# Kernel tuning notes

Measured on AMD Instinct MI355X. Metric: run time of the kernel, lower is better.

Reference implementation:

```python
import jax, jax.numpy as jnp
import numpy as np

ATOMF_LEN = 82
EDGE_DIM = 6
HIDDEN = 10
GNN_DEPTH = 2
N_NODES = 200000
N_EDGES = 6400000


def _lrelu(x):
    return jax.nn.leaky_relu(x, negative_slope=0.1)


def setup_inputs() -> dict:
    key = jax.random.key(0)
    ks = jax.random.split(key, 7)
    vertex = jax.random.normal(ks[0], (N_NODES, ATOMF_LEN), dtype=jnp.float32)
    edge_feat = jax.random.normal(ks[1], (N_EDGES, EDGE_DIM), dtype=jnp.float32)
    src = jax.random.randint(ks[2], (N_EDGES,), 0, N_NODES, dtype=jnp.int32)
    dst = jax.random.randint(ks[3], (N_EDGES,), 0, N_NODES, dtype=jnp.int32)
    # kaiming-uniform-ish init scale (fan_in based)
    weight_init = jax.random.uniform(ks[4], (ATOMF_LEN, HIDDEN), dtype=jnp.float32,
                                     minval=-1.0, maxval=1.0) * (np.sqrt(6.0 / ATOMF_LEN))
    gather_weight = jax.random.uniform(ks[5], (HIDDEN + EDGE_DIM, HIDDEN), dtype=jnp.float32,
                                       minval=-1.0, maxval=1.0) * (np.sqrt(6.0 / (HIDDEN + EDGE_DIM)))
    update_weight = jax.random.uniform(ks[6], (2 * HIDDEN, HIDDEN), dtype=jnp.float32,
                                       minval=-1.0, maxval=1.0) * (np.sqrt(6.0 / (2 * HIDDEN)))
    return {"vertex": vertex, "edge_feat": edge_feat, "src": src, "dst": dst,
            "weight_init": weight_init, "gather_weight": gather_weight,
            "update_weight": update_weight}


def reference(vertex, edge_feat, src, dst, weight_init, gather_weight, update_weight):
    # embedding_: leaky_relu(mm(x, W), 0.1)
    h = _lrelu(vertex @ weight_init)  # [N, HIDDEN]
    n_nodes = vertex.shape[0]
    for _ in range(GNN_DEPTH):
        # gather: per-edge message from source node hidden + edge features
        msg = _lrelu(jnp.concatenate([h[src], edge_feat], axis=1) @ gather_weight)  # [E, HIDDEN]
        # scatter-sum aggregation onto destination nodes
        agg = jax.ops.segment_sum(msg, dst, num_segments=n_nodes)  # [N, HIDDEN]
        # update: combine current hidden with aggregated messages
        h = _lrelu(jnp.concatenate([h, agg], axis=1) @ update_weight)  # [N, HIDDEN]
    return h
```

## Files before the change

### kernel.cpp

```cpp
#include <hip/hip_runtime.h>

#define ATOMF 82
#define EDGE_DIM 6
#define HIDDEN 10
#define ZPAD 16

__device__ __forceinline__ float lrelu(float x) { return x > 0.f ? x : 0.1f * x; }

__device__ __forceinline__ unsigned int f2bf(float f) {
    unsigned int u = __float_as_uint(f);
    return (u + 0x7fffu + ((u >> 16) & 1u)) >> 16;
}
__device__ __forceinline__ float bf2f(unsigned int b) {
    return __uint_as_float(b << 16);
}

__global__ void embed_kernel(const float* __restrict__ vertex,
                             const float* __restrict__ W,
                             const float* __restrict__ GW,
                             float* __restrict__ h, unsigned short* __restrict__ z,
                             int n_nodes) {
    __shared__ float w[ATOMF * HIDDEN];
    __shared__ float gwh[HIDDEN * HIDDEN];
    for (int i = threadIdx.x; i < ATOMF * HIDDEN; i += blockDim.x) w[i] = W[i];
    for (int i = threadIdx.x; i < HIDDEN * HIDDEN; i += blockDim.x) gwh[i] = GW[i];
    __syncthreads();
    int node = blockIdx.x * blockDim.x + threadIdx.x;
    if (node >= n_nodes) return;
    const float2* v = (const float2*)(vertex + (long)node * ATOMF);
    float acc[HIDDEN];
#pragma unroll
    for (int j = 0; j < HIDDEN; j++) acc[j] = 0.f;
#pragma unroll 2
    for (int k2 = 0; k2 < ATOMF / 2; k2++) {
        float2 t = v[k2];
#pragma unroll
        for (int j = 0; j < HIDDEN; j++) acc[j] += t.x * w[(2 * k2) * HIDDEN + j];
#pragma unroll
        for (int j = 0; j < HIDDEN; j++) acc[j] += t.y * w[(2 * k2 + 1) * HIDDEN + j];
    }
    float ho[HIDDEN];
    float* out = h + (long)node * HIDDEN;
#pragma unroll
    for (int j = 0; j < HIDDEN; j++) { ho[j] = lrelu(acc[j]); out[j] = ho[j]; }
    float zv[HIDDEN];
#pragma unroll
    for (int j = 0; j < HIDDEN; j++) zv[j] = 0.f;
#pragma unroll
    for (int k = 0; k < HIDDEN; k++) {
        float x = ho[k];
#pragma unroll
        for (int j = 0; j < HIDDEN; j++) zv[j] += x * gwh[k * HIDDEN + j];
    }
    unsigned int* zq = (unsigned int*)(z + (size_t)node * ZPAD);
    int4 pk;
    pk.x = (int)(f2bf(zv[0]) | (f2bf(zv[1]) << 16));
    pk.y = (int)(f2bf(zv[2]) | (f2bf(zv[3]) << 16));
    pk.z = (int)(f2bf(zv[4]) | (f2bf(zv[5]) << 16));
    pk.w = (int)(f2bf(zv[6]) | (f2bf(zv[7]) << 16));
    *(int4*)zq = pk;
    zq[4] = f2bf(zv[8]) | (f2bf(zv[9]) << 16);
}

__global__ void count_pos_kernel(const int* __restrict__ dst, int* __restrict__ counts,
                                 unsigned short* __restrict__ pos, long n_edges) {
    long e0 = ((long)blockIdx.x * blockDim.x + threadIdx.x) * 4;
    if (e0 + 3 < n_edges) {
        int4 d = *(const int4*)(dst + e0);
        ushort4 p;
        p.x = (unsigned short)atomicAdd(&counts[d.x], 1);
        p.y = (unsigned short)atomicAdd(&counts[d.y], 1);
        p.z = (unsigned short)atomicAdd(&counts[d.z], 1);
        p.w = (unsigned short)atomicAdd(&counts[d.w], 1);
        *(ushort4*)(pos + e0) = p;
    } else {
        for (long e = e0; e < n_edges; e++)
            pos[e] = (unsigned short)atomicAdd(&counts[dst[e]], 1);
    }
}

__global__ __launch_bounds__(1024) void scan_block_sums(const int* __restrict__ counts,
                                                        int* __restrict__ partials, int n) {
    __shared__ int ws[16];
    int i = blockIdx.x * 1024 + threadIdx.x;
    int v = (i < n) ? counts[i] : 0;
    int lane = threadIdx.x & 63, wid = threadIdx.x >> 6;
    int s = v;
#pragma unroll
    for (int off = 32; off > 0; off >>= 1) s += __shfl_down(s, off, 64);
    if (lane == 0) ws[wid] = s;
    __syncthreads();
    if (threadIdx.x == 0) {
        int t = 0;
#pragma unroll
        for (int k = 0; k < 16; k++) t += ws[k];
        partials[blockIdx.x] = t;
    }
}
__global__ __launch_bounds__(1024) void scan_partials(int* __restrict__ partials, int nb) {
    __shared__ int wsum[16];
    int lane = threadIdx.x & 63, wid = threadIdx.x >> 6;
    int v = (threadIdx.x < nb) ? partials[threadIdx.x] : 0;
    int incl = v;
#pragma unroll
    for (int off = 1; off < 64; off <<= 1) {
        int t = __shfl_up(incl, off, 64);
        if (lane >= off) incl += t;
    }
    if (lane == 63) wsum[wid] = incl;
    __syncthreads();
    if (wid == 0 && lane < 16) {
        int wv = wsum[lane];
        int wincl = wv;
#pragma unroll
        for (int off = 1; off < 16; off <<= 1) {
            int t = __shfl_up(wincl, off, 64);
            if (lane >= off) wincl += t;
        }
        wsum[lane] = wincl - wv;
    }
    __syncthreads();
    if (threadIdx.x < nb) partials[threadIdx.x] = wsum[wid] + (incl - v);
}
__global__ __launch_bounds__(1024) void scan_final(const int* __restrict__ counts,
                                                   const int* __restrict__ partials,
                                                   int* __restrict__ offsets, int n) {
    __shared__ int wsum[16];
    int i = blockIdx.x * 1024 + threadIdx.x;
    int v = (i < n) ? counts[i] : 0;
    int lane = threadIdx.x & 63, wid = threadIdx.x >> 6;
    int incl = v;
#pragma unroll
    for (int off = 1; off < 64; off <<= 1) {
        int t = __shfl_up(incl, off, 64);
        if (lane >= off) incl += t;
    }
    if (lane == 63) wsum[wid] = incl;
    __syncthreads();
    if (wid == 0 && lane < 16) {
        int wv = wsum[lane];
        int wincl = wv;
#pragma unroll
        for (int off = 1; off < 16; off <<= 1) {
            int t = __shfl_up(wincl, off, 64);
            if (lane >= off) wincl += t;
        }
        wsum[lane] = wincl - wv;
    }
    __syncthreads();
    if (i <= n) offsets[i] = partials[blockIdx.x] + wsum[wid] + (incl - v);
}

__global__ void scatter_rec_kernel(const int* __restrict__ src, const int* __restrict__ dst,
                                   const float* __restrict__ ef,
                                   const unsigned short* __restrict__ pos,
                                   const int* __restrict__ offsets,
                                   int4* __restrict__ rec, long n_edges) {
    long e = (long)blockIdx.x * blockDim.x + threadIdx.x;
    if (e >= n_edges) return;
    int d = dst[e];
    int q = offsets[d] + (int)pos[e];
    const float2* er = (const float2*)(ef + e * (long)EDGE_DIM);
    float2 a = er[0], b = er[1], c = er[2];
    int4 r;
    r.x = src[e];
    r.y = (int)(f2bf(a.x) | (f2bf(a.y) << 16));
    r.z = (int)(f2bf(b.x) | (f2bf(b.y) << 16));
    r.w = (int)(f2bf(c.x) | (f2bf(c.y) << 16));
    rec[q] = r;
}

__global__ __launch_bounds__(256) void gather_update_kernel(
    const float* __restrict__ h_in, const unsigned short* __restrict__ z_in,
    const int4* __restrict__ rec, const int* __restrict__ offsets,
    const float* __restrict__ GW, const float* __restrict__ UW,
    float* __restrict__ h_out, unsigned short* __restrict__ z_out,
    int n_nodes, int write_z) {
    __shared__ float gwh[HIDDEN * HIDDEN];
    __shared__ float gwe[EDGE_DIM * HIDDEN];
    __shared__ float uw[2 * HIDDEN * HIDDEN];
    for (int i = threadIdx.x; i < HIDDEN * HIDDEN; i += 256) gwh[i] = GW[i];
    for (int i = threadIdx.x; i < EDGE_DIM * HIDDEN; i += 256) gwe[i] = GW[HIDDEN * HIDDEN + i];
    for (int i = threadIdx.x; i < 2 * HIDDEN * HIDDEN; i += 256) uw[i] = UW[i];
    __syncthreads();
    int group = threadIdx.x >> 4;
    int sub = threadIdx.x & 15;
    int node = blockIdx.x * 16 + group;
    if (node >= n_nodes) return;
    int off0 = offsets[node], off1 = offsets[node + 1];
    float acc[HIDDEN];
#pragma unroll
    for (int j = 0; j < HIDDEN; j++) acc[j] = 0.f;
    int p = off0 + sub;
    int4 r;
    if (p < off1) r = rec[p];
    while (p < off1) {
        int pn = p + 16;
        int4 rn = r;
        if (pn < off1) rn = rec[pn];
        const int* zq = (const int*)(z_in + (size_t)r.x * ZPAD);
        int4 za = *(const int4*)zq;
        int zb = zq[4];
        float ef[EDGE_DIM];
        unsigned int u0 = (unsigned int)r.y, u1 = (unsigned int)r.z, u2 = (unsigned int)r.w;
        ef[0] = bf2f(u0 & 0xffffu); ef[1] = bf2f(u0 >> 16);
        ef[2] = bf2f(u1 & 0xffffu); ef[3] = bf2f(u1 >> 16);
        ef[4] = bf2f(u2 & 0xffffu); ef[5] = bf2f(u2 >> 16);
        float m[HIDDEN];
#pragma unroll
        for (int j = 0; j < HIDDEN; j++) m[j] = 0.f;
#pragma unroll
        for (int k = 0; k < EDGE_DIM; k++) {
            float x = ef[k];
#pragma unroll
            for (int j = 0; j < HIDDEN; j++) m[j] += x * gwe[k * HIDDEN + j];
        }
        unsigned int z0 = (unsigned int)za.x, z1 = (unsigned int)za.y;
        unsigned int z2 = (unsigned int)za.z, z3 = (unsigned int)za.w, z4 = (unsigned int)zb;
        acc[0] += lrelu(m[0] + bf2f(z0 & 0xffffu));
        acc[1] += lrelu(m[1] + bf2f(z0 >> 16));
        acc[2] += lrelu(m[2] + bf2f(z1 & 0xffffu));
        acc[3] += lrelu(m[3] + bf2f(z1 >> 16));
        acc[4] += lrelu(m[4] + bf2f(z2 & 0xffffu));
        acc[5] += lrelu(m[5] + bf2f(z2 >> 16));
        acc[6] += lrelu(m[6] + bf2f(z3 & 0xffffu));
        acc[7] += lrelu(m[7] + bf2f(z3 >> 16));
        acc[8] += lrelu(m[8] + bf2f(z4 & 0xffffu));
        acc[9] += lrelu(m[9] + bf2f(z4 >> 16));
        r = rn; p = pn;
    }
#pragma unroll
    for (int j = 0; j < HIDDEN; j++) {
#pragma unroll
        for (int d = 8; d > 0; d >>= 1) acc[j] += __shfl_down(acc[j], d, 16);
    }
    if (sub == 0) {
        float in[2 * HIDDEN];
        const float2* hp = (const float2*)(h_in + (long)node * HIDDEN);
#pragma unroll
        for (int k = 0; k < 5; k++) { float2 t = hp[k]; in[2 * k] = t.x; in[2 * k + 1] = t.y; }
#pragma unroll
        for (int j = 0; j < HIDDEN; j++) in[HIDDEN + j] = acc[j];
        float o[HIDDEN];
#pragma unroll
        for (int j = 0; j < HIDDEN; j++) o[j] = 0.f;
#pragma unroll
        for (int k = 0; k < 2 * HIDDEN; k++) {
            float x = in[k];
#pragma unroll
            for (int j = 0; j < HIDDEN; j++) o[j] += x * uw[k * HIDDEN + j];
        }
        float ho[HIDDEN];
        float* outp = h_out + (long)node * HIDDEN;
#pragma unroll
        for (int j = 0; j < HIDDEN; j++) { ho[j] = lrelu(o[j]); outp[j] = ho[j]; }
        if (write_z) {
            float zv[HIDDEN];
#pragma unroll
            for (int j = 0; j < HIDDEN; j++) zv[j] = 0.f;
#pragma unroll
            for (int k = 0; k < HIDDEN; k++) {
                float x = ho[k];
#pragma unroll
                for (int j = 0; j < HIDDEN; j++) zv[j] += x * gwh[k * HIDDEN + j];
            }
            unsigned int* zq = (unsigned int*)(z_out + (size_t)node * ZPAD);
            int4 pk;
            pk.x = (int)(f2bf(zv[0]) | (f2bf(zv[1]) << 16));
            pk.y = (int)(f2bf(zv[2]) | (f2bf(zv[3]) << 16));
            pk.z = (int)(f2bf(zv[4]) | (f2bf(zv[5]) << 16));
            pk.w = (int)(f2bf(zv[6]) | (f2bf(zv[7]) << 16));
            *(int4*)zq = pk;
            zq[4] = f2bf(zv[8]) | (f2bf(zv[9]) << 16);
        }
    }
}

extern "C" void kernel_launch(void* const* d_in, const int* in_sizes, int n_in,
                              void* d_out, int out_size, void* d_ws, size_t ws_size,
                              hipStream_t stream) {
    const float* vertex    = (const float*)d_in[0];
    const float* edge_feat = (const float*)d_in[1];
    const int*   src       = (const int*)d_in[2];
    const int*   dst       = (const int*)d_in[3];
    const float* w_init    = (const float*)d_in[4];
    const float* gw        = (const float*)d_in[5];
    const float* uw        = (const float*)d_in[6];

    const int  n_nodes = in_sizes[0] / ATOMF;
    const long n_edges = (long)in_sizes[2];
    float* out = (float*)d_out;

    char* ws = (char*)d_ws;
    size_t o = 0;
    auto alloc = [&](size_t bytes) { char* p = ws + o; o = (o + bytes + 255) & ~(size_t)255; return p; };
    int*  counts   = (int*)alloc((size_t)(n_nodes + 1) * sizeof(int));
    int*  offsets  = (int*)alloc((size_t)(n_nodes + 1) * sizeof(int));
    int*  partials = (int*)alloc(2048 * sizeof(int));
    int4* rec      = (int4*)alloc((size_t)n_edges * sizeof(int4));
    size_t pos_bytes = (size_t)n_edges * sizeof(unsigned short);
    size_t tbl_bytes = (size_t)n_nodes * (2 * HIDDEN * sizeof(float) + 2 * ZPAD * sizeof(unsigned short));
    char* overlay = alloc(pos_bytes > tbl_bytes ? pos_bytes : tbl_bytes);
    unsigned short* pos = (unsigned short*)overlay;
    float*          h0  = (float*)overlay;
    float*          h1  = h0 + (size_t)n_nodes * HIDDEN;
    unsigned short* z0  = (unsigned short*)(h1 + (size_t)n_nodes * HIDDEN);
    unsigned short* z1  = z0 + (size_t)n_nodes * ZPAD;
    (void)ws_size;

    const int TB = 256;
    const int node_blocks = (n_nodes + TB - 1) / TB;
    const int edge_blocks = (int)((n_edges + TB - 1) / TB);
    const int cp_blocks   = (int)((n_edges / 4 + TB - 1) / TB);
    const int gu_blocks   = (n_nodes + 15) / 16;
    const int scan_blocks = (n_nodes + 1 + 1023) / 1024;

    hipMemsetAsync(counts, 0, (size_t)(n_nodes + 1) * sizeof(int), stream);
    count_pos_kernel<<<cp_blocks, TB, 0, stream>>>(dst, counts, pos, n_edges);
    scan_block_sums<<<scan_blocks, 1024, 0, stream>>>(counts, partials, n_nodes);
    scan_partials<<<1, 1024, 0, stream>>>(partials, scan_blocks);
    scan_final<<<scan_blocks, 1024, 0, stream>>>(counts, partials, offsets, n_nodes);
    scatter_rec_kernel<<<edge_blocks, TB, 0, stream>>>(src, dst, edge_feat, pos, offsets,
                                                       rec, n_edges);

    embed_kernel<<<node_blocks, TB, 0, stream>>>(vertex, w_init, gw, h0, z0, n_nodes);

    gather_update_kernel<<<gu_blocks, TB, 0, stream>>>(h0, z0, rec, offsets, gw, uw,
                                                       h1, z1, n_nodes, 1);
    gather_update_kernel<<<gu_blocks, TB, 0, stream>>>(h1, z1, rec, offsets, gw, uw,
                                                       out, z0, n_nodes, 0);
}
```

Before: 913.9 us.

## Privatize per-XCD destination counters to keep CSR-build atomics local

The counting pass now gives each XCD (read from the hardware XCC_ID register) its own copy of the per-node counters and issues workgroup-scoped relaxed atomics on that copy. The XCD id is packed into the high bits of the 16-bit position field. The scans sum the eight copies, and the final scan turns each copy into a per-XCD base offset that the scatter pass uses. This targets cross-die coherence traffic and contention on device-scope atomics, at the cost of eight times the counter memory and extra reads during the scan. It relies on per-XCD counts staying below 8192 per node, and on workgroup-scope atomics staying coherent within one XCD's L2.

```diff
diff --git a/kernel.cpp b/kernel.cpp
--- a/kernel.cpp
+++ b/kernel.cpp
@@ -4,6 +4,9 @@
 #define EDGE_DIM 6
 #define HIDDEN 10
 #define ZPAD 16
+#define NXCD 8
+#define POSBITS 13
+#define POSMASK 0x1fff
 
 __device__ __forceinline__ float lrelu(float x) { return x > 0.f ? x : 0.1f * x; }
 
@@ -13,6 +16,12 @@
 }
 __device__ __forceinline__ float bf2f(unsigned int b) {
     return __uint_as_float(b << 16);
+}
+
+__device__ __forceinline__ int xcc_id() {
+    unsigned int x;
+    asm("s_getreg_b32 %0, hwreg(HW_REG_XCC_ID)" : "=s"(x));
+    return (int)(x & (NXCD - 1));
 }
 
 __global__ void embed_kernel(const float* __restrict__ vertex,
@@ -62,28 +71,40 @@
     zq[4] = f2bf(zv[8]) | (f2bf(zv[9]) << 16);
 }
 
-__global__ void count_pos_kernel(const int* __restrict__ dst, int* __restrict__ counts,
-                                 unsigned short* __restrict__ pos, long n_edges) {
+__global__ void count_pos_kernel(const int* __restrict__ dst, int* __restrict__ counts8,
+                                 unsigned short* __restrict__ pos, int n_nodes, long n_edges) {
+    int xcc = xcc_id();
+    int* mycnt = counts8 + (size_t)xcc * (size_t)n_nodes;
+    unsigned int tag = (unsigned int)xcc << POSBITS;
     long e0 = ((long)blockIdx.x * blockDim.x + threadIdx.x) * 4;
     if (e0 + 3 < n_edges) {
         int4 d = *(const int4*)(dst + e0);
         ushort4 p;
-        p.x = (unsigned short)atomicAdd(&counts[d.x], 1);
-        p.y = (unsigned short)atomicAdd(&counts[d.y], 1);
-        p.z = (unsigned short)atomicAdd(&counts[d.z], 1);
-        p.w = (unsigned short)atomicAdd(&counts[d.w], 1);
+        p.x = (unsigned short)(tag | __hip_atomic_fetch_add(&mycnt[d.x], 1, __ATOMIC_RELAXED,
+                                                            __HIP_MEMORY_SCOPE_WORKGROUP));
+        p.y = (unsigned short)(tag | __hip_atomic_fetch_add(&mycnt[d.y], 1, __ATOMIC_RELAXED,
+                                                            __HIP_MEMORY_SCOPE_WORKGROUP));
+        p.z = (unsigned short)(tag | __hip_atomic_fetch_add(&mycnt[d.z], 1, __ATOMIC_RELAXED,
+                                                            __HIP_MEMORY_SCOPE_WORKGROUP));
+        p.w = (unsigned short)(tag | __hip_atomic_fetch_add(&mycnt[d.w], 1, __ATOMIC_RELAXED,
+                                                            __HIP_MEMORY_SCOPE_WORKGROUP));
         *(ushort4*)(pos + e0) = p;
     } else {
         for (long e = e0; e < n_edges; e++)
-            pos[e] = (unsigned short)atomicAdd(&counts[dst[e]], 1);
-    }
-}
-
-__global__ __launch_bounds__(1024) void scan_block_sums(const int* __restrict__ counts,
+            pos[e] = (unsigned short)(tag | __hip_atomic_fetch_add(&mycnt[dst[e]], 1, __ATOMIC_RELAXED,
+                                                                   __HIP_MEMORY_SCOPE_WORKGROUP));
+    }
+}
+
+__global__ __launch_bounds__(1024) void scan_block_sums(const int* __restrict__ counts8,
                                                         int* __restrict__ partials, int n) {
     __shared__ int ws[16];
     int i = blockIdx.x * 1024 + threadIdx.x;
-    int v = (i < n) ? counts[i] : 0;
+    int v = 0;
+    if (i < n) {
+#pragma unroll
+        for (int x = 0; x < NXCD; x++) v += counts8[(size_t)x * n + i];
+    }
     int lane = threadIdx.x & 63, wid = threadIdx.x >> 6;
     int s = v;
 #pragma unroll
@@ -122,12 +143,17 @@
     __syncthreads();
     if (threadIdx.x < nb) partials[threadIdx.x] = wsum[wid] + (incl - v);
 }
-__global__ __launch_bounds__(1024) void scan_final(const int* __restrict__ counts,
+__global__ __launch_bounds__(1024) void scan_final(int* __restrict__ counts8,
                                                    const int* __restrict__ partials,
                                                    int* __restrict__ offsets, int n) {
     __shared__ int wsum[16];
     int i = blockIdx.x * 1024 + threadIdx.x;
-    int v = (i < n) ? counts[i] : 0;
+    int c[NXCD];
+    int v = 0;
+    if (i < n) {
+#pragma unroll
+        for (int x = 0; x < NXCD; x++) { c[x] = counts8[(size_t)x * n + i]; v += c[x]; }
+    }
     int lane = threadIdx.x & 63, wid = threadIdx.x >> 6;
     int incl = v;
 #pragma unroll
@@ -148,18 +174,25 @@
         wsum[lane] = wincl - wv;
     }
     __syncthreads();
-    if (i <= n) offsets[i] = partials[blockIdx.x] + wsum[wid] + (incl - v);
+    int ex = partials[blockIdx.x] + wsum[wid] + (incl - v);
+    if (i < n) {
+        int b = ex;
+#pragma unroll
+        for (int x = 0; x < NXCD; x++) { int cx = c[x]; counts8[(size_t)x * n + i] = b; b += cx; }
+    }
+    if (i <= n) offsets[i] = ex;
 }
 
 __global__ void scatter_rec_kernel(const int* __restrict__ src, const int* __restrict__ dst,
                                    const float* __restrict__ ef,
                                    const unsigned short* __restrict__ pos,
-                                   const int* __restrict__ offsets,
-                                   int4* __restrict__ rec, long n_edges) {
+                                   const int* __restrict__ base8,
+                                   int4* __restrict__ rec, int n_nodes, long n_edges) {
     long e = (long)blockIdx.x * blockDim.x + threadIdx.x;
     if (e >= n_edges) return;
     int d = dst[e];
-    int q = offsets[d] + (int)pos[e];
+    unsigned int p = pos[e];
+    int q = base8[(size_t)(p >> POSBITS) * (size_t)n_nodes + d] + (int)(p & POSMASK);
     const float2* er = (const float2*)(ef + e * (long)EDGE_DIM);
     float2 a = er[0], b = er[1], c = er[2];
     int4 r;
@@ -294,7 +327,7 @@
     char* ws = (char*)d_ws;
     size_t o = 0;
     auto alloc = [&](size_t bytes) { char* p = ws + o; o = (o + bytes + 255) & ~(size_t)255; return p; };
-    int*  counts   = (int*)alloc((size_t)(n_nodes + 1) * sizeof(int));
+    int*  counts8  = (int*)alloc((size_t)NXCD * n_nodes * sizeof(int));
     int*  offsets  = (int*)alloc((size_t)(n_nodes + 1) * sizeof(int));
     int*  partials = (int*)alloc(2048 * sizeof(int));
     int4* rec      = (int4*)alloc((size_t)n_edges * sizeof(int4));
@@ -315,13 +348,13 @@
     const int gu_blocks   = (n_nodes + 15) / 16;
     const int scan_blocks = (n_nodes + 1 + 1023) / 1024;
 
-    hipMemsetAsync(counts, 0, (size_t)(n_nodes + 1) * sizeof(int), stream);
-    count_pos_kernel<<<cp_blocks, TB, 0, stream>>>(dst, counts, pos, n_edges);
-    scan_block_sums<<<scan_blocks, 1024, 0, stream>>>(counts, partials, n_nodes);
+    hipMemsetAsync(counts8, 0, (size_t)NXCD * n_nodes * sizeof(int), stream);
+    count_pos_kernel<<<cp_blocks, TB, 0, stream>>>(dst, counts8, pos, n_nodes, n_edges);
+    scan_block_sums<<<scan_blocks, 1024, 0, stream>>>(counts8, partials, n_nodes);
     scan_partials<<<1, 1024, 0, stream>>>(partials, scan_blocks);
-    scan_final<<<scan_blocks, 1024, 0, stream>>>(counts, partials, offsets, n_nodes);
-    scatter_rec_kernel<<<edge_blocks, TB, 0, stream>>>(src, dst, edge_feat, pos, offsets,
-                                                       rec, n_edges);
+    scan_final<<<scan_blocks, 1024, 0, stream>>>(counts8, partials, offsets, n_nodes);
+    scatter_rec_kernel<<<edge_blocks, TB, 0, stream>>>(src, dst, edge_feat, pos, counts8,
+                                                       rec, n_nodes, n_edges);
 
     embed_kernel<<<node_blocks, TB, 0, stream>>>(vertex, w_init, gw, h0, z0, n_nodes);
 
```

Result: slower. 961.7 us (+5.2%).

## Build CSR via two-pass bucketed radix partition instead of global atomics

Applied to the files above, without the earlier changes.

Replaces the per-edge global atomic counting and random scatter with a two-level partition. Edges are first histogrammed into 256-node buckets with shared-memory atomics and scattered by bucket. Each bucket is then sorted locally in shared memory to produce the CSR offsets and records. This is meant to cut contended global atomics and make the 16-byte record writes more local. In exchange it adds an extra pass over the records and needs extra workspace for the dst2 and rec_a buffers; if the workspace is too small it falls back to the old path.

```diff
diff --git a/kernel.cpp b/kernel.cpp
--- a/kernel.cpp
+++ b/kernel.cpp
@@ -4,6 +4,11 @@
 #define EDGE_DIM 6
 #define HIDDEN 10
 #define ZPAD 16
+
+#define BSHIFT 8
+#define MAXBUCK 1024
+#define NB1 1024
+#define MAXE3 16384
 
 __device__ __forceinline__ float lrelu(float x) { return x > 0.f ? x : 0.1f * x; }
 
@@ -60,6 +65,161 @@
     pk.w = (int)(f2bf(zv[6]) | (f2bf(zv[7]) << 16));
     *(int4*)zq = pk;
     zq[4] = f2bf(zv[8]) | (f2bf(zv[9]) << 16);
+}
+
+__global__ __launch_bounds__(256) void hist_kernel(const int* __restrict__ dst,
+                                                   int* __restrict__ hist,
+                                                   long n_edges, int nbuck) {
+    __shared__ int hl[MAXBUCK];
+    for (int t = threadIdx.x; t < nbuck; t += 256) hl[t] = 0;
+    __syncthreads();
+    long per = (n_edges + gridDim.x - 1) / gridDim.x;
+    long s = (long)blockIdx.x * per;
+    long e = s + per; if (e > n_edges) e = n_edges;
+    for (long i = s + threadIdx.x; i < e; i += 256)
+        atomicAdd(&hl[dst[i] >> BSHIFT], 1);
+    __syncthreads();
+    for (int t = threadIdx.x; t < nbuck; t += 256)
+        hist[(size_t)t * gridDim.x + blockIdx.x] = hl[t];
+}
+
+__global__ __launch_bounds__(1024) void scan_block_sums(const int* __restrict__ in,
+                                                        int* __restrict__ partials, int n) {
+    __shared__ int ws[16];
+    int i = blockIdx.x * 1024 + threadIdx.x;
+    int v = (i < n) ? in[i] : 0;
+    int lane = threadIdx.x & 63, wid = threadIdx.x >> 6;
+    int s = v;
+#pragma unroll
+    for (int off = 32; off > 0; off >>= 1) s += __shfl_down(s, off, 64);
+    if (lane == 0) ws[wid] = s;
+    __syncthreads();
+    if (threadIdx.x == 0) {
+        int t = 0;
+#pragma unroll
+        for (int k = 0; k < 16; k++) t += ws[k];
+        partials[blockIdx.x] = t;
+    }
+}
+__global__ __launch_bounds__(1024) void scan_partials(int* __restrict__ partials, int nb) {
+    __shared__ int wsum[16];
+    int lane = threadIdx.x & 63, wid = threadIdx.x >> 6;
+    int v = (threadIdx.x < nb) ? partials[threadIdx.x] : 0;
+    int incl = v;
+#pragma unroll
+    for (int off = 1; off < 64; off <<= 1) {
+        int t = __shfl_up(incl, off, 64);
+        if (lane >= off) incl += t;
+    }
+    if (lane == 63) wsum[wid] = incl;
+    __syncthreads();
+    if (wid == 0 && lane < 16) {
+        int wv = wsum[lane];
+        int wincl = wv;
+#pragma unroll
+        for (int off = 1; off < 16; off <<= 1) {
+            int t = __shfl_up(wincl, off, 64);
+            if (lane >= off) wincl += t;
+        }
+        wsum[lane] = wincl - wv;
+    }
+    __syncthreads();
+    if (threadIdx.x < nb) partials[threadIdx.x] = wsum[wid] + (incl - v);
+}
+__global__ __launch_bounds__(1024) void scan_final(const int* __restrict__ in,
+                                                   const int* __restrict__ partials,
+                                                   int* __restrict__ out, int n) {
+    __shared__ int wsum[16];
+    int i = blockIdx.x * 1024 + threadIdx.x;
+    int v = (i < n) ? in[i] : 0;
+    int lane = threadIdx.x & 63, wid = threadIdx.x >> 6;
+    int incl = v;
+#pragma unroll
+    for (int off = 1; off < 64; off <<= 1) {
+        int t = __shfl_up(incl, off, 64);
+        if (lane >= off) incl += t;
+    }
+    if (lane == 63) wsum[wid] = incl;
+    __syncthreads();
+    if (wid == 0 && lane < 16) {
+        int wv = wsum[lane];
+        int wincl = wv;
+#pragma unroll
+        for (int off = 1; off < 16; off <<= 1) {
+            int t = __shfl_up(wincl, off, 64);
+            if (lane >= off) wincl += t;
+        }
+        wsum[lane] = wincl - wv;
+    }
+    __syncthreads();
+    if (i <= n) out[i] = partials[blockIdx.x] + wsum[wid] + (incl - v);
+}
+
+__global__ __launch_bounds__(256) void part_scatter_kernel(
+    const int* __restrict__ src, const int* __restrict__ dst,
+    const float* __restrict__ ef, const int* __restrict__ base,
+    int4* __restrict__ rec_a, int* __restrict__ dst2,
+    long n_edges, int nbuck) {
+    __shared__ int cur[MAXBUCK];
+    for (int t = threadIdx.x; t < nbuck; t += 256)
+        cur[t] = base[(size_t)t * gridDim.x + blockIdx.x];
+    __syncthreads();
+    long per = (n_edges + gridDim.x - 1) / gridDim.x;
+    long s = (long)blockIdx.x * per;
+    long e = s + per; if (e > n_edges) e = n_edges;
+    for (long i = s + threadIdx.x; i < e; i += 256) {
+        int d = dst[i];
+        int slot = atomicAdd(&cur[d >> BSHIFT], 1);
+        const float2* er = (const float2*)(ef + i * (long)EDGE_DIM);
+        float2 fa = er[0], fb = er[1], fc = er[2];
+        int4 r;
+        r.x = src[i];
+        r.y = (int)(f2bf(fa.x) | (f2bf(fa.y) << 16));
+        r.z = (int)(f2bf(fb.x) | (f2bf(fb.y) << 16));
+        r.w = (int)(f2bf(fc.x) | (f2bf(fc.y) << 16));
+        rec_a[slot] = r;
+        dst2[slot] = d;
+    }
+}
+
+__global__ __launch_bounds__(256) void bucket_csr_kernel(
+    const int* __restrict__ base, const int* __restrict__ dst2,
+    const int4* __restrict__ rec_a, int4* __restrict__ rec_b,
+    int* __restrict__ offsets, int n_nodes) {
+    __shared__ unsigned char lid[MAXE3];
+    __shared__ int cnt[1 << BSHIFT];
+    __shared__ int excl_s[1 << BSHIFT];
+    __shared__ int cursor[1 << BSHIFT];
+    int b = blockIdx.x;
+    int S = base[(size_t)b * NB1];
+    int E = base[(size_t)(b + 1) * NB1];
+    int node0 = b << BSHIFT;
+    int nn = n_nodes - node0; if (nn > (1 << BSHIFT)) nn = 1 << BSHIFT;
+    cnt[threadIdx.x] = 0;
+    __syncthreads();
+    int ne = E - S;
+    bool fit = (ne <= MAXE3);
+    for (int i = threadIdx.x; i < ne; i += 256) {
+        int l = dst2[S + i] - node0;
+        if (fit) lid[i] = (unsigned char)l;
+        atomicAdd(&cnt[l], 1);
+    }
+    __syncthreads();
+    if (threadIdx.x == 0) {
+        int run = 0;
+#pragma unroll 4
+        for (int l = 0; l < (1 << BSHIFT); l++) { excl_s[l] = run; run += cnt[l]; }
+    }
+    __syncthreads();
+    if ((int)threadIdx.x < nn) offsets[node0 + threadIdx.x] = S + excl_s[threadIdx.x];
+    cursor[threadIdx.x] = excl_s[threadIdx.x];
+    if (b == (int)gridDim.x - 1 && threadIdx.x == 0) offsets[n_nodes] = E;
+    __syncthreads();
+    for (int i = threadIdx.x; i < ne; i += 256) {
+        int l = fit ? (int)lid[i] : (dst2[S + i] - node0);
+        int r = atomicAdd(&cursor[l], 1);
+        rec_b[S + r] = rec_a[S + i];
+    }
 }
 
 __global__ void count_pos_kernel(const int* __restrict__ dst, int* __restrict__ counts,
@@ -78,79 +238,6 @@
             pos[e] = (unsigned short)atomicAdd(&counts[dst[e]], 1);
     }
 }
-
-__global__ __launch_bounds__(1024) void scan_block_sums(const int* __restrict__ counts,
-                                                        int* __restrict__ partials, int n) {
-    __shared__ int ws[16];
-    int i = blockIdx.x * 1024 + threadIdx.x;
-    int v = (i < n) ? counts[i] : 0;
-    int lane = threadIdx.x & 63, wid = threadIdx.x >> 6;
-    int s = v;
-#pragma unroll
-    for (int off = 32; off > 0; off >>= 1) s += __shfl_down(s, off, 64);
-    if (lane == 0) ws[wid] = s;
-    __syncthreads();
-    if (threadIdx.x == 0) {
-        int t = 0;
-#pragma unroll
-        for (int k = 0; k < 16; k++) t += ws[k];
-        partials[blockIdx.x] = t;
-    }
-}
-__global__ __launch_bounds__(1024) void scan_partials(int* __restrict__ partials, int nb) {
-    __shared__ int wsum[16];
-    int lane = threadIdx.x & 63, wid = threadIdx.x >> 6;
-    int v = (threadIdx.x < nb) ? partials[threadIdx.x] : 0;
-    int incl = v;
-#pragma unroll
-    for (int off = 1; off < 64; off <<= 1) {
-        int t = __shfl_up(incl, off, 64);
-        if (lane >= off) incl += t;
-    }
-    if (lane == 63) wsum[wid] = incl;
-    __syncthreads();
-    if (wid == 0 && lane < 16) {
-        int wv = wsum[lane];
-        int wincl = wv;
-#pragma unroll
-        for (int off = 1; off < 16; off <<= 1) {
-            int t = __shfl_up(wincl, off, 64);
-            if (lane >= off) wincl += t;
-        }
-        wsum[lane] = wincl - wv;
-    }
-    __syncthreads();
-    if (threadIdx.x < nb) partials[threadIdx.x] = wsum[wid] + (incl - v);
-}
-__global__ __launch_bounds__(1024) void scan_final(const int* __restrict__ counts,
-                                                   const int* __restrict__ partials,
-                                                   int* __restrict__ offsets, int n) {
-    __shared__ int wsum[16];
-    int i = blockIdx.x * 1024 + threadIdx.x;
-    int v = (i < n) ? counts[i] : 0;
-    int lane = threadIdx.x & 63, wid = threadIdx.x >> 6;
-    int incl = v;
-#pragma unroll
-    for (int off = 1; off < 64; off <<= 1) {
-        int t = __shfl_up(incl, off, 64);
-        if (lane >= off) incl += t;
-    }
-    if (lane == 63) wsum[wid] = incl;
-    __syncthreads();
-    if (wid == 0 && lane < 16) {
-        int wv = wsum[lane];
-        int wincl = wv;
-#pragma unroll
-        for (int off = 1; off < 16; off <<= 1) {
-            int t = __shfl_up(wincl, off, 64);
-            if (lane >= off) wincl += t;
-        }
-        wsum[lane] = wincl - wv;
-    }
-    __syncthreads();
-    if (i <= n) offsets[i] = partials[blockIdx.x] + wsum[wid] + (incl - v);
-}
-
 __global__ void scatter_rec_kernel(const int* __restrict__ src, const int* __restrict__ dst,
                                    const float* __restrict__ ef,
                                    const unsigned short* __restrict__ pos,
@@ -161,12 +248,12 @@
     int d = dst[e];
     int q = offsets[d] + (int)pos[e];
     const float2* er = (const float2*)(ef + e * (long)EDGE_DIM);
-    float2 a = er[0], b = er[1], c = er[2];
+    float2 fa = er[0], fb = er[1], fc = er[2];
     int4 r;
     r.x = src[e];
-    r.y = (int)(f2bf(a.x) | (f2bf(a.y) << 16));
-    r.z = (int)(f2bf(b.x) | (f2bf(b.y) << 16));
-    r.w = (int)(f2bf(c.x) | (f2bf(c.y) << 16));
+    r.y = (int)(f2bf(fa.x) | (f2bf(fa.y) << 16));
+    r.z = (int)(f2bf(fb.x) | (f2bf(fb.y) << 16));
+    r.w = (int)(f2bf(fc.x) | (f2bf(fc.y) << 16));
     rec[q] = r;
 }
 
@@ -291,42 +378,85 @@
     const long n_edges = (long)in_sizes[2];
     float* out = (float*)d_out;
 
+    const int TB = 256;
+    const int node_blocks = (n_nodes + TB - 1) / TB;
+    const int gu_blocks   = (n_nodes + 15) / 16;
+
+    const int nbuck = (n_nodes + (1 << BSHIFT) - 1) >> BSHIFT;
+    const long m = (long)nbuck * NB1;
+    const int scanb_m = (int)((m + 1 + 1023) / 1024);
+
+    size_t tbl_bytes = (size_t)n_nodes * (2 * HIDDEN * sizeof(float) + 2 * ZPAD * sizeof(unsigned short));
+    size_t rec_bytes = (size_t)n_edges * sizeof(int4);
+
+    auto al = [](size_t x) { return (x + 255) & ~(size_t)255; };
+    size_t need_new = al(m * 4) + al((m + 1) * 4) + al(2048 * 4) +
+                      al((size_t)(n_nodes + 1) * 4) + al(rec_bytes) +
+                      al(rec_bytes > tbl_bytes ? rec_bytes : tbl_bytes) +
+                      al((size_t)n_edges * 4);
+
     char* ws = (char*)d_ws;
     size_t o = 0;
     auto alloc = [&](size_t bytes) { char* p = ws + o; o = (o + bytes + 255) & ~(size_t)255; return p; };
-    int*  counts   = (int*)alloc((size_t)(n_nodes + 1) * sizeof(int));
-    int*  offsets  = (int*)alloc((size_t)(n_nodes + 1) * sizeof(int));
-    int*  partials = (int*)alloc(2048 * sizeof(int));
-    int4* rec      = (int4*)alloc((size_t)n_edges * sizeof(int4));
-    size_t pos_bytes = (size_t)n_edges * sizeof(unsigned short);
-    size_t tbl_bytes = (size_t)n_nodes * (2 * HIDDEN * sizeof(float) + 2 * ZPAD * sizeof(unsigned short));
-    char* overlay = alloc(pos_bytes > tbl_bytes ? pos_bytes : tbl_bytes);
-    unsigned short* pos = (unsigned short*)overlay;
-    float*          h0  = (float*)overlay;
-    float*          h1  = h0 + (size_t)n_nodes * HIDDEN;
-    unsigned short* z0  = (unsigned short*)(h1 + (size_t)n_nodes * HIDDEN);
-    unsigned short* z1  = z0 + (size_t)n_nodes * ZPAD;
+
+    if (nbuck <= MAXBUCK && scanb_m <= 1024 && ws_size >= need_new) {
+        int*  hist     = (int*)alloc(m * 4);
+        int*  base     = (int*)alloc((m + 1) * 4);
+        int*  partials = (int*)alloc(2048 * 4);
+        int*  offsets  = (int*)alloc((size_t)(n_nodes + 1) * 4);
+        int4* rec_b    = (int4*)alloc(rec_bytes);
+        char* ovl      = alloc(rec_bytes > tbl_bytes ? rec_bytes : tbl_bytes);
+        int4* rec_a    = (int4*)ovl;
+        int*  dst2     = (int*)alloc((size_t)n_edges * 4);
+        float*          h0 = (float*)ovl;
+        float*          h1 = h0 + (size_t)n_nodes * HIDDEN;
+        unsigned short* z0 = (unsigned short*)(h1 + (size_t)n_nodes * HIDDEN);
+        unsigned short* z1 = z0 + (size_t)n_nodes * ZPAD;
+
+        hipMemsetAsync(hist, 0, m * 4, stream);
+        hist_kernel<<<NB1, 256, 0, stream>>>(dst, hist, n_edges, nbuck);
+        scan_block_sums<<<scanb_m, 1024, 0, stream>>>(hist, partials, (int)m);
+        scan_partials<<<1, 1024, 0, stream>>>(partials, scanb_m);
+        scan_final<<<scanb_m, 1024, 0, stream>>>(hist, partials, base, (int)m);
+        part_scatter_kernel<<<NB1, 256, 0, stream>>>(src, dst, edge_feat, base,
+                                                     rec_a, dst2, n_edges, nbuck);
+        bucket_csr_kernel<<<nbuck, 256, 0, stream>>>(base, dst2, rec_a, rec_b,
+                                                     offsets, n_nodes);
+
+        embed_kernel<<<node_blocks, TB, 0, stream>>>(vertex, w_init, gw, h0, z0, n_nodes);
+        gather_update_kernel<<<gu_blocks, TB, 0, stream>>>(h0, z0, rec_b, offsets, gw, uw,
+                                                           h1, z1, n_nodes, 1);
+        gather_update_kernel<<<gu_blocks, TB, 0, stream>>>(h1, z1, rec_b, offsets, gw, uw,
+                                                           out, z0, n_nodes, 0);
+    } else {
+        int*  counts   = (int*)alloc((size_t)(n_nodes + 1) * 4);
+        int*  offsets  = (int*)alloc((size_t)(n_nodes + 1) * 4);
+        int*  partials = (int*)alloc(2048 * 4);
+        int4* rec      = (int4*)alloc(rec_bytes);
+        size_t pos_bytes = (size_t)n_edges * sizeof(unsigned short);
+        char* overlay = alloc(pos_bytes > tbl_bytes ? pos_bytes : tbl_bytes);
+        unsigned short* pos = (unsigned short*)overlay;
+        float*          h0  = (float*)overlay;
+        float*          h1  = h0 + (size_t)n_nodes * HIDDEN;
+        unsigned short* z0  = (unsigned short*)(h1 + (size_t)n_nodes * HIDDEN);
+        unsigned short* z1  = z0 + (size_t)n_nodes * ZPAD;
+
+        const int edge_blocks = (int)((n_edges + TB - 1) / TB);
+        const int cp_blocks   = (int)((n_edges / 4 + TB - 1) / TB);
+        const int scan_blocks = (n_nodes + 1 + 1023) / 1024;
+
+        hipMemsetAsync(counts, 0, (size_t)(n_nodes + 1) * 4, stream);
+        count_pos_kernel<<<cp_blocks, TB, 0, stream>>>(dst, counts, pos, n_edges);
+        scan_block_sums<<<scan_blocks, 1024, 0, stream>>>(counts, partials, n_nodes);
+        scan_partials<<<1, 1024, 0, stream>>>(partials, scan_blocks);
+        scan_final<<<scan_blocks, 1024, 0, stream>>>(counts, partials, offsets, n_nodes);
+        scatter_rec_kernel<<<edge_blocks, TB, 0, stream>>>(src, dst, edge_feat, pos, offsets,
+                                                           rec, n_edges);
+        embed_kernel<<<node_blocks, TB, 0, stream>>>(vertex, w_init, gw, h0, z0, n_nodes);
+        gather_update_kernel<<<gu_blocks, TB, 0, stream>>>(h0, z0, rec, offsets, gw, uw,
+                                                           h1, z1, n_nodes, 1);
+        gather_update_kernel<<<gu_blocks, TB, 0, stream>>>(h1, z1, rec, offsets, gw, uw,
+                                                           out, z0, n_nodes, 0);
+    }
     (void)ws_size;
-
-    const int TB = 256;
-    const int node_blocks = (n_nodes + TB - 1) / TB;
-    const int edge_blocks = (int)((n_edges + TB - 1) / TB);
-    const int cp_blocks   = (int)((n_edges / 4 + TB - 1) / TB);
-    const int gu_blocks   = (n_nodes + 15) / 16;
-    const int scan_blocks = (n_nodes + 1 + 1023) / 1024;
-
-    hipMemsetAsync(counts, 0, (size_t)(n_nodes + 1) * sizeof(int), stream);
-    count_pos_kernel<<<cp_blocks, TB, 0, stream>>>(dst, counts, pos, n_edges);
-    scan_block_sums<<<scan_blocks, 1024, 0, stream>>>(counts, partials, n_nodes);
-    scan_partials<<<1, 1024, 0, stream>>>(partials, scan_blocks);
-    scan_final<<<scan_blocks, 1024, 0, stream>>>(counts, partials, offsets, n_nodes);
-    scatter_rec_kernel<<<edge_blocks, TB, 0, stream>>>(src, dst, edge_feat, pos, offsets,
-                                                       rec, n_edges);
-
-    embed_kernel<<<node_blocks, TB, 0, stream>>>(vertex, w_init, gw, h0, z0, n_nodes);
-
-    gather_update_kernel<<<gu_blocks, TB, 0, stream>>>(h0, z0, rec, offsets, gw, uw,
-                                                       h1, z1, n_nodes, 1);
-    gather_update_kernel<<<gu_blocks, TB, 0, stream>>>(h1, z1, rec, offsets, gw, uw,
-                                                       out, z0, n_nodes, 0);
-}
+}
```

Result: faster. 878.9 us (-3.8%).
